# Kernel tuning notes

Hardware: AMD Instinct MI355X
Metric: run time of the kernel (lower is better)

## Reference

```python
import jax, jax.numpy as jnp
import numpy as np

N_WORDS = 262144
N_TAGS = 512
BDIM = 768
MDIM = 128


def setup_inputs() -> dict:
    key = jax.random.key(0)
    k1, k2, k3, k4, k5, k6 = jax.random.split(key, 6)
    scale = 1.0 / np.sqrt(BDIM)
    return {
        "tags_embed": jax.random.normal(k1, (N_TAGS, BDIM), dtype=jnp.float32),
        "words_embed": jax.random.normal(k2, (N_WORDS, BDIM), dtype=jnp.float32),
        "tags_W": jax.random.normal(k3, (MDIM, BDIM), dtype=jnp.float32) * scale,
        "tags_b": jax.random.normal(k4, (MDIM,), dtype=jnp.float32) * scale,
        "words_W": jax.random.normal(k5, (MDIM, BDIM), dtype=jnp.float32) * scale,
        "words_b": jax.random.normal(k6, (MDIM,), dtype=jnp.float32) * scale,
    }


def reference(tags_embed, words_embed, tags_W, tags_b, words_W, words_b):
    # Linear projections into the metric space: [T, M] and [N, M]
    tags_m = tags_embed @ tags_W.T + tags_b
    words_m = words_embed @ words_W.T + words_b
    # Pairwise squared Euclidean distances via ||w||^2 + ||t||^2 - 2 w.t
    # (same math as the expand-subtract-pow-sum, GEMM-based instead)
    w_sq = jnp.sum(words_m * words_m, axis=1, keepdims=True)  # [N, 1]
    t_sq = jnp.sum(tags_m * tags_m, axis=1)[None, :]          # [1, T]
    distances = w_sq + t_sq - 2.0 * (words_m @ tags_m.T)      # [N, T]
    logits = -distances
    log_pred_y = jax.nn.log_softmax(logits, axis=1)
    pred_y = jax.nn.softmax(logits, axis=1)
    return (log_pred_y, pred_y)
```

## Files before the change

kernel.cpp:

```cpp
#include <hip/hip_runtime.h>

#define N_WORDS 262144
#define N_TAGS  512
#define BDIM    768
#define MDIM    128
#define KS      32
#define NSL     (BDIM / KS)
#define BW      32
#define EPAD    40

typedef __attribute__((ext_vector_type(8))) short  bf16x8;
typedef __attribute__((ext_vector_type(4))) float  f32x4;

__device__ inline unsigned bf16_1(float a) {
    union { float f; unsigned u; } ua; ua.f = a;
    unsigned x = ua.u;
    x += 0x7fffu + ((x >> 16) & 1u);
    return x >> 16;
}
__device__ inline unsigned bf16_2(float a, float b) {
    union { float f; unsigned u; } ua, ub; ua.f = a; ub.f = b;
    unsigned x = ua.u, y = ub.u;
    x += 0x7fffu + ((x >> 16) & 1u);
    y += 0x7fffu + ((y >> 16) & 1u);
    return (x >> 16) | (y & 0xffff0000u);
}

__global__ __launch_bounds__(128) void tags_kernel(
    const float* __restrict__ tags_embed, const float* __restrict__ tags_W,
    const float* __restrict__ tags_b, const float* __restrict__ words_b,
    unsigned short* __restrict__ Tbf, float* __restrict__ cvec)
{
    __shared__ __align__(16) float sE[BDIM];
    __shared__ float red[128];
    const int t = blockIdx.x;
    const int m = threadIdx.x;

    for (int i = m; i < BDIM; i += 128) sE[i] = tags_embed[(size_t)t * BDIM + i];
    __syncthreads();

    float acc = tags_b[m];
    const float* Wr = tags_W + (size_t)m * BDIM;
    #pragma unroll 8
    for (int b = 0; b < BDIM; b += 4) {
        float4 w4 = *reinterpret_cast<const float4*>(Wr + b);
        float4 e4 = *reinterpret_cast<const float4*>(&sE[b]);
        acc += w4.x * e4.x + w4.y * e4.y + w4.z * e4.z + w4.w * e4.w;
    }
    Tbf[(size_t)t * MDIM + m] = (unsigned short)bf16_1(2.0f * acc);

    red[m] = acc * (2.0f * words_b[m] - acc);
    __syncthreads();
    for (int s = 64; s > 0; s >>= 1) {
        if (m < s) red[m] += red[m + s];
        __syncthreads();
    }
    if (m == 0) cvec[t] = red[0];
}

__global__ __launch_bounds__(256) void wt_kernel(
    const float* __restrict__ W, unsigned short* __restrict__ Wtbf)
{
    __shared__ float sT[32][33];
    const int bm = blockIdx.x & 3, bk = blockIdx.x >> 2;
    const int m0 = bm * 32, k0 = bk * 32;
    const int r = threadIdx.x >> 3, c = threadIdx.x & 7;

    f32x4 w4 = *reinterpret_cast<const f32x4*>(W + (size_t)(m0 + r) * BDIM + k0 + c * 4);
    sT[r][c * 4 + 0] = w4.x;  sT[r][c * 4 + 1] = w4.y;
    sT[r][c * 4 + 2] = w4.z;  sT[r][c * 4 + 3] = w4.w;
    __syncthreads();

    unsigned lo = bf16_2(sT[c * 4 + 0][r], sT[c * 4 + 1][r]);
    unsigned hi = bf16_2(sT[c * 4 + 2][r], sT[c * 4 + 3][r]);
    unsigned long long p = ((unsigned long long)hi << 32) | lo;
    *reinterpret_cast<unsigned long long*>(Wtbf + (size_t)(k0 + r) * MDIM + m0 + c * 4) = p;
}

__global__ __launch_bounds__(64) void gt_kernel(
    const unsigned short* __restrict__ Wtbf, const unsigned short* __restrict__ Tbf,
    unsigned short* __restrict__ GtSl)
{
    const int kt = blockIdx.x % 48, tg = blockIdx.x / 48;
    const int k0 = kt * 16, t0 = tg * 64;
    const int n = threadIdx.x & 15, q = threadIdx.x >> 4;

    bf16x8 a[4];
    #pragma unroll
    for (int ks = 0; ks < 4; ++ks)
        a[ks] = *reinterpret_cast<const bf16x8*>(
            Wtbf + (size_t)(k0 + n) * MDIM + ks * 32 + q * 8);

    const int s2  = kt >> 1;
    const int off = (kt & 1) * 16 + 4 * q;

    #pragma unroll
    for (int tt = 0; tt < 4; ++tt) {
        f32x4 acc = (f32x4){0.f, 0.f, 0.f, 0.f};
        #pragma unroll
        for (int ks = 0; ks < 4; ++ks) {
            bf16x8 b = *reinterpret_cast<const bf16x8*>(
                Tbf + (size_t)(t0 + tt * 16 + n) * MDIM + ks * 32 + q * 8);
            acc = __builtin_amdgcn_mfma_f32_16x16x32_bf16(a[ks], b, acc, 0, 0, 0);
        }
        unsigned lo = bf16_2(acc.x, acc.y);
        unsigned hi = bf16_2(acc.z, acc.w);
        unsigned long long p = ((unsigned long long)hi << 32) | lo;
        *reinterpret_cast<unsigned long long*>(
            GtSl + (size_t)s2 * (N_TAGS * KS) + (size_t)(t0 + tt * 16 + n) * KS + off) = p;
    }
}

__global__ __launch_bounds__(512, 4) void main_kernel(
    const float* __restrict__ embed,
    const unsigned short* __restrict__ GtSl,
    const float* __restrict__ cvec,
    float* __restrict__ out_logp, float* __restrict__ out_p)
{
    __shared__ __align__(16) unsigned short sE[2][BW * EPAD];
    __shared__ float sMx[8][BW];
    __shared__ float sSm[8][BW];

    const int tid  = threadIdx.x;
    const int lane = tid & 63;
    const int v    = tid >> 6;
    const int n    = lane & 15;
    const int q    = lane >> 4;
    const int we   = tid >> 4;
    const int kp   = tid & 15;
    const int w0   = blockIdx.x * BW;

    unsigned pk[24];
    {
        const float* eS = embed + (size_t)(w0 + we) * BDIM + kp * 4;
        f32x4 e[12];
        #pragma unroll
        for (int r = 0; r < 12; ++r)
            e[r] = *reinterpret_cast<const f32x4*>(eS + r * 64);
        #pragma unroll
        for (int r = 0; r < 12; ++r) {
            pk[2 * r]     = bf16_2(e[r].x, e[r].y);
            pk[2 * r + 1] = bf16_2(e[r].z, e[r].w);
        }
    }

    if (kp < 8)
        *reinterpret_cast<unsigned long long*>(&sE[0][we * EPAD + (kp & 7) * 4]) =
            ((unsigned long long)pk[1] << 32) | pk[0];

    const unsigned short* Ab = GtSl + (size_t)(v * 64 + n) * KS + q * 8;
    bf16x8 aC[4], aN[4];
    #pragma unroll
    for (int mt = 0; mt < 4; ++mt)
        aC[mt] = *reinterpret_cast<const bf16x8*>(Ab + mt * 512);

    asm volatile("s_waitcnt lgkmcnt(0)\n\ts_barrier" ::: "memory");

    f32x4 acc[4][2];
    #pragma unroll
    for (int mt = 0; mt < 4; ++mt) {
        acc[mt][0] = (f32x4){0.f, 0.f, 0.f, 0.f};
        acc[mt][1] = (f32x4){0.f, 0.f, 0.f, 0.f};
    }

    #pragma unroll
    for (int s = 0; s < NSL; ++s) {
        const int cur = s & 1;

        if (s + 1 < NSL) {
            if ((kp >> 3) == ((s + 1) & 1)) {
                const int r = (s + 1) >> 1;
                *reinterpret_cast<unsigned long long*>(
                    &sE[cur ^ 1][we * EPAD + (kp & 7) * 4]) =
                    ((unsigned long long)pk[2 * r + 1] << 32) | pk[2 * r];
            }
            #pragma unroll
            for (int mt = 0; mt < 4; ++mt)
                aN[mt] = *reinterpret_cast<const bf16x8*>(
                    Ab + (size_t)(s + 1) * (N_TAGS * KS) + mt * 512);
        }

        bf16x8 b0 = *reinterpret_cast<const bf16x8*>(&sE[cur][n * EPAD + q * 8]);
        bf16x8 b1 = *reinterpret_cast<const bf16x8*>(&sE[cur][(16 + n) * EPAD + q * 8]);
        #pragma unroll
        for (int mt = 0; mt < 4; ++mt) {
            acc[mt][0] = __builtin_amdgcn_mfma_f32_16x16x32_bf16(aC[mt], b0, acc[mt][0], 0, 0, 0);
            acc[mt][1] = __builtin_amdgcn_mfma_f32_16x16x32_bf16(aC[mt], b1, acc[mt][1], 0, 0, 0);
        }

        if (s + 1 < NSL) {
            asm volatile("s_waitcnt lgkmcnt(0)\n\ts_barrier" ::: "memory");
            #pragma unroll
            for (int mt = 0; mt < 4; ++mt) aC[mt] = aN[mt];
        }
    }

    #pragma unroll
    for (int mt = 0; mt < 4; ++mt) {
        f32x4 c4 = *reinterpret_cast<const f32x4*>(cvec + v * 64 + mt * 16 + 4 * q);
        acc[mt][0] += c4;
        acc[mt][1] += c4;
    }

    float mx[2], sm[2];
    #pragma unroll
    for (int wt = 0; wt < 2; ++wt) {
        float m = -3.0e38f;
        #pragma unroll
        for (int mt = 0; mt < 4; ++mt)
            m = fmaxf(m, fmaxf(fmaxf(acc[mt][wt].x, acc[mt][wt].y),
                               fmaxf(acc[mt][wt].z, acc[mt][wt].w)));
        m = fmaxf(m, __shfl_xor(m, 16, 64));
        m = fmaxf(m, __shfl_xor(m, 32, 64));
        mx[wt] = m;
        float s = 0.f;
        #pragma unroll
        for (int mt = 0; mt < 4; ++mt)
            s += __expf(acc[mt][wt].x - m) + __expf(acc[mt][wt].y - m)
               + __expf(acc[mt][wt].z - m) + __expf(acc[mt][wt].w - m);
        s += __shfl_xor(s, 16, 64);
        s += __shfl_xor(s, 32, 64);
        sm[wt] = s;
    }
    if (q == 0) {
        sMx[v][n]      = mx[0];
        sMx[v][16 + n] = mx[1];
        sSm[v][n]      = sm[0];
        sSm[v][16 + n] = sm[1];
    }
    __syncthreads();

    #pragma unroll
    for (int wt = 0; wt < 2; ++wt) {
        const int wd = wt * 16 + n;
        float M = sMx[0][wd];
        #pragma unroll
        for (int u = 1; u < 8; ++u) M = fmaxf(M, sMx[u][wd]);
        float S = 0.f;
        #pragma unroll
        for (int u = 0; u < 8; ++u) S += sSm[u][wd] * __expf(sMx[u][wd] - M);
        const float neg = M + __logf(S);

        const size_t row = (size_t)(w0 + wd) * N_TAGS + v * 64 + 4 * q;
        #pragma unroll
        for (int mt = 0; mt < 4; ++mt) {
            f32x4 lp, pp;
            lp.x = acc[mt][wt].x - neg;  pp.x = __expf(lp.x);
            lp.y = acc[mt][wt].y - neg;  pp.y = __expf(lp.y);
            lp.z = acc[mt][wt].z - neg;  pp.z = __expf(lp.z);
            lp.w = acc[mt][wt].w - neg;  pp.w = __expf(lp.w);
            *reinterpret_cast<f32x4*>(out_logp + row + mt * 16) = lp;
            *reinterpret_cast<f32x4*>(out_p    + row + mt * 16) = pp;
        }
    }
}

extern "C" void kernel_launch(void* const* d_in, const int* in_sizes, int n_in,
                              void* d_out, int out_size, void* d_ws, size_t ws_size,
                              hipStream_t stream) {
    const float* tags_embed  = (const float*)d_in[0];
    const float* words_embed = (const float*)d_in[1];
    const float* tags_W      = (const float*)d_in[2];
    const float* tags_b      = (const float*)d_in[3];
    const float* words_W     = (const float*)d_in[4];
    const float* words_b     = (const float*)d_in[5];

    float* out_logp = (float*)d_out;
    float* out_p    = out_logp + (size_t)N_WORDS * N_TAGS;

    unsigned short* Tbf  = (unsigned short*)d_ws;
    float*          cvec = (float*)(Tbf + (size_t)N_TAGS * MDIM);
    unsigned short* Wtbf = (unsigned short*)(cvec + N_TAGS);
    unsigned short* GtSl = Wtbf + (size_t)BDIM * MDIM;

    tags_kernel<<<N_TAGS, 128, 0, stream>>>(tags_embed, tags_W, tags_b, words_b, Tbf, cvec);
    wt_kernel<<<96, 256, 0, stream>>>(words_W, Wtbf);
    gt_kernel<<<384, 64, 0, stream>>>(Wtbf, Tbf, GtSl);
    main_kernel<<<N_WORDS / BW, 512, 0, stream>>>(
        words_embed, GtSl, cvec, out_logp, out_p);
}
```

Baseline: 643.7 us.

## Stage full embedding row tile in LDS and prefetch tag slices two ahead

```diff
diff --git a/kernel.cpp b/kernel.cpp
--- a/kernel.cpp
+++ b/kernel.cpp
@@ -7,7 +7,7 @@
 #define KS      32
 #define NSL     (BDIM / KS)
 #define BW      32
-#define EPAD    40
+#define EPAD    776
 
 typedef __attribute__((ext_vector_type(8))) short  bf16x8;
 typedef __attribute__((ext_vector_type(4))) float  f32x4;
@@ -117,7 +117,7 @@
     const float* __restrict__ cvec,
     float* __restrict__ out_logp, float* __restrict__ out_p)
 {
-    __shared__ __align__(16) unsigned short sE[2][BW * EPAD];
+    __shared__ __align__(16) unsigned short sE[BW * EPAD];
     __shared__ float sMx[8][BW];
     __shared__ float sSm[8][BW];
 
@@ -126,35 +126,30 @@
     const int v    = tid >> 6;
     const int n    = lane & 15;
     const int q    = lane >> 4;
-    const int we   = tid >> 4;
-    const int kp   = tid & 15;
     const int w0   = blockIdx.x * BW;
 
-    unsigned pk[24];
+    const unsigned short* Ab = GtSl + (size_t)(v * 64 + n) * KS + q * 8;
+
+    bf16x8 A0[4], A1[4], A2[4];
+    #pragma unroll
+    for (int mt = 0; mt < 4; ++mt) {
+        A0[mt] = *reinterpret_cast<const bf16x8*>(Ab + mt * (16 * KS));
+        A1[mt] = *reinterpret_cast<const bf16x8*>(Ab + (size_t)(N_TAGS * KS) + mt * (16 * KS));
+    }
+
     {
-        const float* eS = embed + (size_t)(w0 + we) * BDIM + kp * 4;
-        f32x4 e[12];
-        #pragma unroll
-        for (int r = 0; r < 12; ++r)
-            e[r] = *reinterpret_cast<const f32x4*>(eS + r * 64);
+        const int w = tid >> 4, seg = tid & 15;
+        const float* eS = embed + (size_t)(w0 + w) * BDIM + seg * 4;
         #pragma unroll
         for (int r = 0; r < 12; ++r) {
-            pk[2 * r]     = bf16_2(e[r].x, e[r].y);
-            pk[2 * r + 1] = bf16_2(e[r].z, e[r].w);
+            f32x4 e = *reinterpret_cast<const f32x4*>(eS + r * 64);
+            unsigned lo = bf16_2(e.x, e.y), hi = bf16_2(e.z, e.w);
+            *reinterpret_cast<unsigned long long*>(
+                &sE[w * EPAD + seg * 4 + r * 64]) =
+                ((unsigned long long)hi << 32) | lo;
         }
     }
-
-    if (kp < 8)
-        *reinterpret_cast<unsigned long long*>(&sE[0][we * EPAD + (kp & 7) * 4]) =
-            ((unsigned long long)pk[1] << 32) | pk[0];
-
-    const unsigned short* Ab = GtSl + (size_t)(v * 64 + n) * KS + q * 8;
-    bf16x8 aC[4], aN[4];
-    #pragma unroll
-    for (int mt = 0; mt < 4; ++mt)
-        aC[mt] = *reinterpret_cast<const bf16x8*>(Ab + mt * 512);
-
-    asm volatile("s_waitcnt lgkmcnt(0)\n\ts_barrier" ::: "memory");
+    __syncthreads();
 
     f32x4 acc[4][2];
     #pragma unroll
@@ -163,37 +158,40 @@
         acc[mt][1] = (f32x4){0.f, 0.f, 0.f, 0.f};
     }
 
-    #pragma unroll
-    for (int s = 0; s < NSL; ++s) {
-        const int cur = s & 1;
-
-        if (s + 1 < NSL) {
-            if ((kp >> 3) == ((s + 1) & 1)) {
-                const int r = (s + 1) >> 1;
-                *reinterpret_cast<unsigned long long*>(
-                    &sE[cur ^ 1][we * EPAD + (kp & 7) * 4]) =
-                    ((unsigned long long)pk[2 * r + 1] << 32) | pk[2 * r];
-            }
-            #pragma unroll
-            for (int mt = 0; mt < 4; ++mt)
-                aN[mt] = *reinterpret_cast<const bf16x8*>(
-                    Ab + (size_t)(s + 1) * (N_TAGS * KS) + mt * 512);
-        }
-
-        bf16x8 b0 = *reinterpret_cast<const bf16x8*>(&sE[cur][n * EPAD + q * 8]);
-        bf16x8 b1 = *reinterpret_cast<const bf16x8*>(&sE[cur][(16 + n) * EPAD + q * 8]);
-        #pragma unroll
-        for (int mt = 0; mt < 4; ++mt) {
-            acc[mt][0] = __builtin_amdgcn_mfma_f32_16x16x32_bf16(aC[mt], b0, acc[mt][0], 0, 0, 0);
-            acc[mt][1] = __builtin_amdgcn_mfma_f32_16x16x32_bf16(aC[mt], b1, acc[mt][1], 0, 0, 0);
-        }
-
-        if (s + 1 < NSL) {
-            asm volatile("s_waitcnt lgkmcnt(0)\n\ts_barrier" ::: "memory");
-            #pragma unroll
-            for (int mt = 0; mt < 4; ++mt) aC[mt] = aN[mt];
-        }
-    }
+#define SLICE(sv, C, P, DO_PF)                                               \
+    {                                                                        \
+        if (DO_PF) {                                                         \
+            _Pragma("unroll")                                                \
+            for (int mt = 0; mt < 4; ++mt)                                   \
+                P[mt] = *reinterpret_cast<const bf16x8*>(                    \
+                    Ab + (size_t)((sv) + 2) * (N_TAGS * KS) + mt * (16 * KS)); \
+        }                                                                    \
+        bf16x8 b0 = *reinterpret_cast<const bf16x8*>(                        \
+            &sE[n * EPAD + (sv) * 32 + q * 8]);                              \
+        bf16x8 b1 = *reinterpret_cast<const bf16x8*>(                        \
+            &sE[(16 + n) * EPAD + (sv) * 32 + q * 8]);                       \
+        __builtin_amdgcn_s_setprio(1);                                       \
+        _Pragma("unroll")                                                    \
+        for (int mt = 0; mt < 4; ++mt) {                                     \
+            acc[mt][0] = __builtin_amdgcn_mfma_f32_16x16x32_bf16(            \
+                C[mt], b0, acc[mt][0], 0, 0, 0);                             \
+            acc[mt][1] = __builtin_amdgcn_mfma_f32_16x16x32_bf16(            \
+                C[mt], b1, acc[mt][1], 0, 0, 0);                             \
+        }                                                                    \
+        __builtin_amdgcn_s_setprio(0);                                       \
+    }
+
+    #pragma unroll 1
+    for (int j = 0; j < 7; ++j) {
+        const int s = 3 * j;
+        SLICE(s,     A0, A2, 1)
+        SLICE(s + 1, A1, A0, 1)
+        SLICE(s + 2, A2, A1, 1)
+    }
+    SLICE(21, A0, A2, 1)
+    SLICE(22, A1, A0, 0)
+    SLICE(23, A2, A0, 0)
+#undef SLICE
 
     #pragma unroll
     for (int mt = 0; mt < 4; ++mt) {
```

Result: slower. 682.1 us (+6.0%).
